# Performance work log

Hardware: AMD Instinct MI355X
Metric: run time of the kernel (lower is better)

The kernel has to match this reference:

```python
import jax, jax.numpy as jnp
import numpy as np

D_MODEL = 1024
D_FF = 4096
N_EXPERTS = 8
TOP_K = 2

def setup_inputs() -> dict:
    key = jax.random.key(0)
    ks = jax.random.split(key, 8)
    s = 0.02
    return {
        "x": jax.random.normal(ks[0], (4, 2048, D_MODEL), dtype=jnp.float32),
        "W1": jax.random.normal(ks[1], (N_EXPERTS, D_MODEL, D_FF), dtype=jnp.float32) * s,
        "b1": jnp.zeros((N_EXPERTS, D_FF), dtype=jnp.float32),
        "W2": jax.random.normal(ks[2], (N_EXPERTS, D_FF, D_MODEL), dtype=jnp.float32) * s,
        "b2": jnp.zeros((N_EXPERTS, D_MODEL), dtype=jnp.float32),
        "Wg": jax.random.normal(ks[3], (D_MODEL, N_EXPERTS), dtype=jnp.float32) * s,
        "bg": jnp.zeros((N_EXPERTS,), dtype=jnp.float32),
    }

def reference(x, W1, b1, W2, b2, Wg, bg):
    B, S, D = x.shape
    # Gating network
    gate_logits = jnp.einsum('bsd,de->bse', x, Wg) + bg
    gate_probs = jax.nn.softmax(gate_logits, axis=-1)  # (B,S,E)
    # Top-k routing on softmax probs (matches torch.topk(F.softmax(logits)))
    top_k_probs, top_k_indices = jax.lax.top_k(gate_probs, TOP_K)  # (B,S,k)
    T = B * S
    x_flat = x.reshape(T, D)
    idx_flat = top_k_indices.reshape(T, TOP_K)
    prob_flat = top_k_probs.reshape(T, TOP_K)
    # Per-token combine weight for each expert: sum of top-k probs routed to it
    # combine[t, e] = sum_j prob_flat[t, j] * (idx_flat[t, j] == e)
    onehot = jax.nn.one_hot(idx_flat, N_EXPERTS, dtype=x.dtype)  # (T,k,E)
    combine = jnp.einsum('tk,tke->te', prob_flat, onehot)  # (T,E)
    out = jnp.zeros((T, D), dtype=x.dtype)
    for e in range(N_EXPERTS):  # static small loop over experts
        h = jax.nn.relu(x_flat @ W1[e] + b1[e])  # (T, d_ff)
        y = h @ W2[e] + b2[e]                    # (T, d_model)
        out = out + combine[:, e:e+1] * y
    return out.reshape(B, S, D), gate_probs
```

## Files before the change

kernel.cpp:

```cpp
#include <hip/hip_runtime.h>

#define D_MODEL 1024
#define D_FF    4096
#define N_EXP   8
#define BM 256
#define BN 256
#define BK 64

typedef __attribute__((ext_vector_type(8))) short bf16x8;
typedef __attribute__((ext_vector_type(4))) float f32x4;
typedef unsigned int u32;

__device__ __forceinline__ unsigned short f2bf(float f) {
  union { float f; unsigned u; } v; v.f = f;
  unsigned r = v.u + 0x7FFFu + ((v.u >> 16) & 1u);
  return (unsigned short)(r >> 16);
}

__device__ __forceinline__ void gl_lds16(const void* g, void* l) {
  __builtin_amdgcn_global_load_lds((const __attribute__((address_space(1))) u32*)g,
                                   (__attribute__((address_space(3))) u32*)l, 16, 0, 0);
}

__global__ void convert_x_kernel(const float* __restrict__ x,
                                 unsigned short* __restrict__ xb, int total8) {
  int i = blockIdx.x * blockDim.x + threadIdx.x;
  if (i >= total8) return;
  const float4* src = (const float4*)x + (size_t)i * 2;
  float4 a = src[0], b = src[1];
  ushort4 lo, hi;
  lo.x = f2bf(a.x); lo.y = f2bf(a.y); lo.z = f2bf(a.z); lo.w = f2bf(a.w);
  hi.x = f2bf(b.x); hi.y = f2bf(b.y); hi.z = f2bf(b.z); hi.w = f2bf(b.w);
  ushort4* dst = (ushort4*)xb + (size_t)i * 2;
  dst[0] = lo; dst[1] = hi;
}

__global__ __launch_bounds__(256)
void transpose_convert_kernel(const float* __restrict__ src, unsigned short* __restrict__ dst,
                              int Ksub, int Nsrc, int k0, int n0, int Nchunk,
                              unsigned long long eStride) {
  __shared__ unsigned short s[64][65];
  int e = blockIdx.z;
  int kb = blockIdx.x * 64, nb = blockIdx.y * 64;
  const float* se = src + (size_t)e * eStride;
  unsigned short* de = dst + (size_t)e * Nchunk * Ksub;
  int tid = threadIdx.x;
  int lk = tid >> 4, ln = (tid & 15) * 4;
  #pragma unroll
  for (int p = 0; p < 4; p++) {
    int k = lk + p * 16;
    float4 v = *(const float4*)(se + (size_t)(k0 + kb + k) * Nsrc + (n0 + nb + ln));
    s[ln + 0][k] = f2bf(v.x);
    s[ln + 1][k] = f2bf(v.y);
    s[ln + 2][k] = f2bf(v.z);
    s[ln + 3][k] = f2bf(v.w);
  }
  __syncthreads();
  #pragma unroll
  for (int c = 0; c < 2; c++) {
    int id = tid + c * 256;
    int n = id >> 3, kc = id & 7;
    unsigned short u[8];
    #pragma unroll
    for (int j = 0; j < 8; j++) u[j] = s[n][kc * 8 + j];
    *(uint4*)(de + (size_t)(nb + n) * Ksub + kb + kc * 8) = *(const uint4*)u;
  }
}

__global__ void gating_kernel(const float* __restrict__ x,
                              const float* __restrict__ Wg,
                              const float* __restrict__ bg,
                              float* __restrict__ gate_out,
                              int* __restrict__ cnt,
                              int* __restrict__ tokIdx,
                              float* __restrict__ tokW, int T) {
  int wv = threadIdx.x >> 6, lane = threadIdx.x & 63;
  int t = blockIdx.x * 4 + wv;
  if (t >= T) return;
  const float* xr = x + (size_t)t * D_MODEL + lane * 16;
  float acc[N_EXP];
  #pragma unroll
  for (int e = 0; e < N_EXP; e++) acc[e] = 0.f;
  #pragma unroll
  for (int q = 0; q < 4; q++) {
    float4 xv = *(const float4*)(xr + q * 4);
    #pragma unroll
    for (int r = 0; r < 4; r++) {
      float xs = ((const float*)&xv)[r];
      const float* wrow = Wg + (size_t)(lane * 16 + q * 4 + r) * N_EXP;
      float4 wa = *(const float4*)wrow;
      float4 wb = *(const float4*)(wrow + 4);
      acc[0] += xs * wa.x; acc[1] += xs * wa.y; acc[2] += xs * wa.z; acc[3] += xs * wa.w;
      acc[4] += xs * wb.x; acc[5] += xs * wb.y; acc[6] += xs * wb.z; acc[7] += xs * wb.w;
    }
  }
  #pragma unroll
  for (int off = 32; off > 0; off >>= 1) {
    #pragma unroll
    for (int e = 0; e < N_EXP; e++) acc[e] += __shfl_xor(acc[e], off);
  }
  if (lane == 0) {
    float l[N_EXP], p[N_EXP];
    float m = -1e30f;
    #pragma unroll
    for (int e = 0; e < N_EXP; e++) { l[e] = acc[e] + bg[e]; m = fmaxf(m, l[e]); }
    float s = 0.f;
    #pragma unroll
    for (int e = 0; e < N_EXP; e++) { p[e] = __expf(l[e] - m); s += p[e]; }
    float inv = 1.f / s;
    #pragma unroll
    for (int e = 0; e < N_EXP; e++) { p[e] *= inv; gate_out[(size_t)t * N_EXP + e] = p[e]; }
    int e1 = 0;
    #pragma unroll
    for (int e = 1; e < N_EXP; e++) if (p[e] > p[e1]) e1 = e;
    int e2 = (e1 == 0) ? 1 : 0;
    #pragma unroll
    for (int e = 0; e < N_EXP; e++) if (e != e1 && p[e] > p[e2]) e2 = e;
    int pos = atomicAdd(cnt + e1, 1);
    tokIdx[(size_t)e1 * T + pos] = t; tokW[(size_t)e1 * T + pos] = p[e1];
    pos = atomicAdd(cnt + e2, 1);
    tokIdx[(size_t)e2 * T + pos] = t; tokW[(size_t)e2 * T + pos] = p[e2];
  }
}

__global__ void schedule_kernel(const int* __restrict__ cnt, int* __restrict__ meta,
                                int* __restrict__ tE, int* __restrict__ tB,
                                int* __restrict__ tV, int T, int maxTiles) {
  if (threadIdx.x != 0 || blockIdx.x != 0) return;
  int t = 0;
  for (int e = 0; e < N_EXP; e++) {
    int c = cnt[e];
    for (int r = 0; r < c && t < maxTiles; r += BM) {
      tE[t] = e; tB[t] = e * T + r; tV[t] = min(BM, c - r); t++;
    }
  }
  meta[0] = t;
}

#define STAGE(bufbase, kt) do { \
    _Pragma("unroll") for (int c_ = 0; c_ < 4; c_++) { \
      gl_lds16(srcA[c_] + (size_t)(kt) * BK, (bufbase) + (w * 32 + c_ * 8) * 64); \
      gl_lds16(srcB[c_] + (size_t)(kt) * BK, (bufbase) + 16384 + (w * 32 + c_ * 8) * 64); } \
  } while (0)

#define RD_A(cur, qm) { _Pragma("unroll") for (int m_ = 0; m_ < 4; m_++) { \
    int row_ = (qm) * 128 + wm64 + m_ * 16 + l15; \
    _Pragma("unroll") for (int kk_ = 0; kk_ < 2; kk_++) \
      a[m_][kk_] = *(const bf16x8*)&(cur)[row_ * 64 + (((kk_ * 4 + l4 + row_) & 7) << 3)]; } }

#define RD_B(cur, qn, bb) { _Pragma("unroll") for (int n_ = 0; n_ < 2; n_++) { \
    int rb_ = (qn) * 128 + wn32 + n_ * 16 + l15; \
    _Pragma("unroll") for (int kk_ = 0; kk_ < 2; kk_++) \
      bb[n_][kk_] = *(const bf16x8*)&(cur)[16384 + rb_ * 64 + (((kk_ * 4 + l4 + rb_) & 7) << 3)]; } }

#define MQ(qm, qn, bb) { _Pragma("unroll") for (int m_ = 0; m_ < 4; m_++) \
    _Pragma("unroll") for (int n_ = 0; n_ < 2; n_++) { \
      acc[qm][qn][m_][n_] = __builtin_amdgcn_mfma_f32_16x16x32_bf16(a[m_][0], bb[n_][0], acc[qm][qn][m_][n_], 0, 0, 0); \
      acc[qm][qn][m_][n_] = __builtin_amdgcn_mfma_f32_16x16x32_bf16(a[m_][1], bb[n_][1], acc[qm][qn][m_][n_], 0, 0, 0); } }

#define KLOOP(NT) \
  STAGE(As, 0); \
  asm volatile("s_waitcnt vmcnt(0)" ::: "memory"); \
  __builtin_amdgcn_sched_barrier(0); \
  __builtin_amdgcn_s_barrier(); \
  __builtin_amdgcn_sched_barrier(0); \
  for (int kt = 0; kt < (NT); kt++) { \
    unsigned short* cur = As + (kt & 1) * 32768; \
    unsigned short* nxt = As + ((kt + 1) & 1) * 32768; \
    if (kt + 1 < (NT)) STAGE(nxt, kt + 1); \
    __builtin_amdgcn_sched_barrier(0); \
    RD_A(cur, 0); RD_B(cur, 0, b0); RD_B(cur, 1, b1); \
    MQ(0, 0, b0); MQ(0, 1, b1); \
    RD_A(cur, 1); \
    MQ(1, 1, b1); MQ(1, 0, b0); \
    __builtin_amdgcn_sched_barrier(0); \
    asm volatile("s_waitcnt vmcnt(0)" ::: "memory"); \
    __builtin_amdgcn_sched_barrier(0); \
    __builtin_amdgcn_s_barrier(); \
    __builtin_amdgcn_sched_barrier(0); \
  }

#define ACC_INIT() f32x4 acc[2][2][4][2]; \
  _Pragma("unroll") for (int qm = 0; qm < 2; qm++) \
    _Pragma("unroll") for (int qn = 0; qn < 2; qn++) \
      _Pragma("unroll") for (int m = 0; m < 4; m++) \
        _Pragma("unroll") for (int n = 0; n < 2; n++) acc[qm][qn][m][n] = (f32x4){0.f, 0.f, 0.f, 0.f};

__global__ __launch_bounds__(512, 2)
void gemm1_kernel(const unsigned short* __restrict__ xb,
                  const unsigned short* __restrict__ w1t,
                  const float* __restrict__ b1,
                  const int* __restrict__ meta,
                  const int* __restrict__ tE, const int* __restrict__ tB,
                  const int* __restrict__ tV, const int* __restrict__ tokIdx,
                  unsigned short* __restrict__ hbuf, int FFC, int chunk_off, int ncolLog2) {
  __shared__ unsigned short As[65536];

  int total = gridDim.x;
  int L = blockIdx.x;
  int q = total >> 3, r8 = total & 7;
  int xcd = L & 7, idx = L >> 3;
  int work = (xcd < r8) ? (xcd * (q + 1) + idx) : (r8 * (q + 1) + (xcd - r8) * q + idx);
  int ncol = 1 << ncolLog2;
  int tile = work >> ncolLog2;
  int cb = work & (ncol - 1);
  if (tile >= meta[0]) return;
  int e = tE[tile], base = tB[tile], valid = tV[tile];
  int tid = threadIdx.x;

  int w = tid >> 6, lane = tid & 63;
  int wm = w >> 2, wn = w & 3;
  int wm64 = wm * 64, wn32 = wn * 32;
  int l15 = lane & 15, l4 = lane >> 4;
  int sr = lane >> 3, scg = lane & 7;

  const unsigned short* panel = w1t + (size_t)e * FFC * D_MODEL;
  const unsigned short* srcA[4];
  const unsigned short* srcB[4];
  #pragma unroll
  for (int c = 0; c < 4; c++) {
    int r = w * 32 + c * 8 + sr;
    int rc = r < valid ? r : valid - 1;
    int tok = tokIdx[base + rc];
    int swz = ((scg - r) & 7) << 3;
    srcA[c] = xb + (size_t)tok * D_MODEL + swz;
    srcB[c] = panel + (size_t)(cb * BN + r) * D_MODEL + swz;
  }

  ACC_INIT();
  bf16x8 a[4][2], b0[2][2], b1f[2][2];
  #define b1 b1f
  KLOOP(D_MODEL / BK);
  #undef b1

  const float* b1e = b1 + (size_t)e * D_FF + chunk_off + cb * BN;
  #pragma unroll
  for (int qn = 0; qn < 2; qn++)
    #pragma unroll
    for (int n = 0; n < 2; n++) {
      int colL = qn * 128 + wn32 + n * 16 + l15;
      float bias = b1e[colL];
      #pragma unroll
      for (int qm = 0; qm < 2; qm++)
        #pragma unroll
        for (int m = 0; m < 4; m++)
          #pragma unroll
          for (int r = 0; r < 4; r++) {
            int row = qm * 128 + wm64 + m * 16 + l4 * 4 + r;
            float v = acc[qm][qn][m][n][r] + bias;
            v = v > 0.f ? v : 0.f;
            hbuf[(size_t)(tile * BM + row) * FFC + cb * BN + colL] = f2bf(v);
          }
    }
}

__global__ __launch_bounds__(512, 2)
void gemm2_kernel(const unsigned short* __restrict__ hbuf,
                  const unsigned short* __restrict__ w2t,
                  const float* __restrict__ b2,
                  const int* __restrict__ meta,
                  const int* __restrict__ tE, const int* __restrict__ tB,
                  const int* __restrict__ tV, const int* __restrict__ tokIdx,
                  const float* __restrict__ tokW,
                  float* __restrict__ out, int FFC, int chunk) {
  __shared__ unsigned short As[65536];

  int total = gridDim.x;
  int L = blockIdx.x;
  int q = total >> 3, r8 = total & 7;
  int xcd = L & 7, idx = L >> 3;
  int work = (xcd < r8) ? (xcd * (q + 1) + idx) : (r8 * (q + 1) + (xcd - r8) * q + idx);
  int tile = work >> 3;
  int cb = (work >> 1) & 3;
  int ks = work & 1;
  if (tile >= meta[0]) return;
  int e = tE[tile], base = tB[tile], valid = tV[tile];
  int tid = threadIdx.x;

  int w = tid >> 6, lane = tid & 63;
  int wm = w >> 2, wn = w & 3;
  int wm64 = wm * 64, wn32 = wn * 32;
  int l15 = lane & 15, l4 = lane >> 4;
  int sr = lane >> 3, scg = lane & 7;

  const int nt = FFC / BK / 2;
  const int ksOff = ks * nt * BK;

  const unsigned short* panel = w2t + (size_t)e * D_MODEL * FFC;
  const unsigned short* srcA[4];
  const unsigned short* srcB[4];
  #pragma unroll
  for (int c = 0; c < 4; c++) {
    int r = w * 32 + c * 8 + sr;
    int swz = ((scg - r) & 7) << 3;
    srcA[c] = hbuf + (size_t)(tile * BM + r) * FFC + ksOff + swz;
    srcB[c] = panel + (size_t)(cb * BN + r) * FFC + ksOff + swz;
  }

  ACC_INIT();
  bf16x8 a[4][2], b0[2][2], b1[2][2];
  KLOOP(nt);

  int addBias = (chunk == 0 && ks == 0) ? 1 : 0;
  #pragma unroll
  for (int qn = 0; qn < 2; qn++)
    #pragma unroll
    for (int n = 0; n < 2; n++) {
      int colg = cb * BN + qn * 128 + wn32 + n * 16 + l15;
      float bias = addBias ? b2[(size_t)e * D_MODEL + colg] : 0.f;
      #pragma unroll
      for (int qm = 0; qm < 2; qm++)
        #pragma unroll
        for (int m = 0; m < 4; m++)
          #pragma unroll
          for (int r = 0; r < 4; r++) {
            int row = qm * 128 + wm64 + m * 16 + l4 * 4 + r;
            if (row < valid) {
              float wgt = tokW[base + row];
              int tok = tokIdx[base + row];
              float v = (acc[qm][qn][m][n][r] + bias) * wgt;
              atomicAdd(out + (size_t)tok * D_MODEL + colg, v);
            }
          }
    }
}

extern "C" void kernel_launch(void* const* d_in, const int* in_sizes, int n_in,
                              void* d_out, int out_size, void* d_ws, size_t ws_size,
                              hipStream_t stream) {
  const float* x  = (const float*)d_in[0];
  const float* W1 = (const float*)d_in[1];
  const float* b1 = (const float*)d_in[2];
  const float* W2 = (const float*)d_in[3];
  const float* b2 = (const float*)d_in[4];
  const float* Wg = (const float*)d_in[5];
  const float* bg = (const float*)d_in[6];

  int T = in_sizes[0] / D_MODEL;
  float* out = (float*)d_out;
  float* gate_out = out + (size_t)T * D_MODEL;

  char* ws = (char*)d_ws;
  int* cnt  = (int*)(ws + 0);
  int* meta = (int*)(ws + 64);
  int* tE   = (int*)(ws + 128);
  int* tB   = (int*)(ws + 1024);
  int* tV   = (int*)(ws + 2048);
  size_t off = 4096;
  int* tokIdx = (int*)(ws + off);   off += (size_t)N_EXP * T * 4;
  float* tokW = (float*)(ws + off); off += (size_t)N_EXP * T * 4;
  unsigned short* xb = (unsigned short*)(ws + off); off += (size_t)T * D_MODEL * 2;
  off = (off + 255) & ~(size_t)255;

  int maxTiles = (2 * T) / BM + N_EXP;
  int FFC = D_FF;
  while (FFC > 256 &&
         off + (size_t)FFC * (16384 + 16384 + (size_t)maxTiles * BM * 2) > ws_size)
    FFC >>= 1;

  unsigned short* w1t = (unsigned short*)(ws + off); off += (size_t)FFC * 16384;
  unsigned short* w2t = (unsigned short*)(ws + off); off += (size_t)FFC * 16384;
  unsigned short* h   = (unsigned short*)(ws + off);

  hipMemsetAsync(d_out, 0, (size_t)T * D_MODEL * sizeof(float), stream);
  hipMemsetAsync(cnt, 0, N_EXP * sizeof(int), stream);

  int total8 = T * D_MODEL / 8;
  convert_x_kernel<<<(total8 + 255) / 256, 256, 0, stream>>>(x, xb, total8);
  gating_kernel<<<(T + 3) / 4, 256, 0, stream>>>(x, Wg, bg, gate_out, cnt, tokIdx, tokW, T);
  schedule_kernel<<<1, 64, 0, stream>>>(cnt, meta, tE, tB, tV, T, maxTiles);

  int ncol1 = FFC / BN;
  int ncol1Log2 = __builtin_ctz(ncol1);
  for (int c = 0; c * FFC < D_FF; c++) {
    transpose_convert_kernel<<<dim3(D_MODEL / 64, FFC / 64, N_EXP), 256, 0, stream>>>(
        W1, w1t, D_MODEL, D_FF, 0, c * FFC, FFC, (unsigned long long)D_MODEL * D_FF);
    transpose_convert_kernel<<<dim3(FFC / 64, D_MODEL / 64, N_EXP), 256, 0, stream>>>(
        W2, w2t, FFC, D_MODEL, c * FFC, 0, D_MODEL, (unsigned long long)D_FF * D_MODEL);
    gemm1_kernel<<<maxTiles * ncol1, 512, 0, stream>>>(
        xb, w1t, b1, meta, tE, tB, tV, tokIdx, h, FFC, c * FFC, ncol1Log2);
    gemm2_kernel<<<maxTiles * (D_MODEL / BN) * 2, 512, 0, stream>>>(
        h, w2t, b2, meta, tE, tB, tV, tokIdx, tokW, out, FFC, c);
  }
}
```

Baseline: 836.2 us.

## Fuse x conversion into gating, repack transpose, split-K 4 in gemm2, tweak scheduling

Folds the fp32-to-bf16 conversion of x into the gating kernel so x is read once, and removes a launch. The weight transpose now packs pairs of bf16 into 32-bit LDS words to cut LDS traffic. gemm2 splits K four ways instead of two and caches token indices and weights in LDS. The K loops drop sched_barriers in favour of s_setprio, and launch bounds move to one block per CU. More split-K means more atomic adds to the output, and the lower occupancy hint may change register allocation.

```diff
diff --git a/kernel.cpp b/kernel.cpp
--- a/kernel.cpp
+++ b/kernel.cpp
@@ -22,48 +22,41 @@
                                    (__attribute__((address_space(3))) u32*)l, 16, 0, 0);
 }
 
-__global__ void convert_x_kernel(const float* __restrict__ x,
-                                 unsigned short* __restrict__ xb, int total8) {
-  int i = blockIdx.x * blockDim.x + threadIdx.x;
-  if (i >= total8) return;
-  const float4* src = (const float4*)x + (size_t)i * 2;
-  float4 a = src[0], b = src[1];
-  ushort4 lo, hi;
-  lo.x = f2bf(a.x); lo.y = f2bf(a.y); lo.z = f2bf(a.z); lo.w = f2bf(a.w);
-  hi.x = f2bf(b.x); hi.y = f2bf(b.y); hi.z = f2bf(b.z); hi.w = f2bf(b.w);
-  ushort4* dst = (ushort4*)xb + (size_t)i * 2;
-  dst[0] = lo; dst[1] = hi;
-}
-
 __global__ __launch_bounds__(256)
 void transpose_convert_kernel(const float* __restrict__ src, unsigned short* __restrict__ dst,
                               int Ksub, int Nsrc, int k0, int n0, int Nchunk,
                               unsigned long long eStride) {
-  __shared__ unsigned short s[64][65];
+  __shared__ u32 s32k[32][65];
   int e = blockIdx.z;
   int kb = blockIdx.x * 64, nb = blockIdx.y * 64;
-  const float* se = src + (size_t)e * eStride;
-  unsigned short* de = dst + (size_t)e * Nchunk * Ksub;
+  const float* se = src + (size_t)e * eStride + (size_t)(k0 + kb) * Nsrc + (n0 + nb);
+  unsigned short* de = dst + (size_t)e * Nchunk * Ksub + (size_t)nb * Ksub + kb;
   int tid = threadIdx.x;
-  int lk = tid >> 4, ln = (tid & 15) * 4;
-  #pragma unroll
-  for (int p = 0; p < 4; p++) {
-    int k = lk + p * 16;
-    float4 v = *(const float4*)(se + (size_t)(k0 + kb + k) * Nsrc + (n0 + nb + ln));
-    s[ln + 0][k] = f2bf(v.x);
-    s[ln + 1][k] = f2bf(v.y);
-    s[ln + 2][k] = f2bf(v.z);
-    s[ln + 3][k] = f2bf(v.w);
+  int kh = tid >> 4;
+  int n4 = (tid & 15) * 4;
+  #pragma unroll
+  for (int p = 0; p < 2; p++) {
+    int k = kh * 2 + p * 32;
+    float4 v0 = *(const float4*)(se + (size_t)k * Nsrc + n4);
+    float4 v1 = *(const float4*)(se + (size_t)(k + 1) * Nsrc + n4);
+    #pragma unroll
+    for (int j = 0; j < 4; j++) {
+      u32 pk = (u32)f2bf(((const float*)&v0)[j]) |
+               ((u32)f2bf(((const float*)&v1)[j]) << 16);
+      s32k[k >> 1][n4 + j] = pk;
+    }
   }
   __syncthreads();
   #pragma unroll
   for (int c = 0; c < 2; c++) {
     int id = tid + c * 256;
     int n = id >> 3, kc = id & 7;
-    unsigned short u[8];
-    #pragma unroll
-    for (int j = 0; j < 8; j++) u[j] = s[n][kc * 8 + j];
-    *(uint4*)(de + (size_t)(nb + n) * Ksub + kb + kc * 8) = *(const uint4*)u;
+    uint4 o;
+    o.x = s32k[kc * 4 + 0][n];
+    o.y = s32k[kc * 4 + 1][n];
+    o.z = s32k[kc * 4 + 2][n];
+    o.w = s32k[kc * 4 + 3][n];
+    *(uint4*)(de + (size_t)n * Ksub + kc * 8) = o;
   }
 }
 
@@ -71,6 +64,7 @@
                               const float* __restrict__ Wg,
                               const float* __restrict__ bg,
                               float* __restrict__ gate_out,
+                              unsigned short* __restrict__ xb,
                               int* __restrict__ cnt,
                               int* __restrict__ tokIdx,
                               float* __restrict__ tokW, int T) {
@@ -81,9 +75,12 @@
   float acc[N_EXP];
   #pragma unroll
   for (int e = 0; e < N_EXP; e++) acc[e] = 0.f;
+  ushort4 xc[4];
   #pragma unroll
   for (int q = 0; q < 4; q++) {
     float4 xv = *(const float4*)(xr + q * 4);
+    xc[q].x = f2bf(xv.x); xc[q].y = f2bf(xv.y);
+    xc[q].z = f2bf(xv.z); xc[q].w = f2bf(xv.w);
     #pragma unroll
     for (int r = 0; r < 4; r++) {
       float xs = ((const float*)&xv)[r];
@@ -94,6 +91,9 @@
       acc[4] += xs * wb.x; acc[5] += xs * wb.y; acc[6] += xs * wb.z; acc[7] += xs * wb.w;
     }
   }
+  unsigned short* xbr = xb + (size_t)t * D_MODEL + lane * 16;
+  #pragma unroll
+  for (int q = 0; q < 4; q++) *(ushort4*)(xbr + q * 4) = xc[q];
   #pragma unroll
   for (int off = 32; off > 0; off >>= 1) {
     #pragma unroll
@@ -161,23 +161,21 @@
 #define KLOOP(NT) \
   STAGE(As, 0); \
   asm volatile("s_waitcnt vmcnt(0)" ::: "memory"); \
-  __builtin_amdgcn_sched_barrier(0); \
   __builtin_amdgcn_s_barrier(); \
-  __builtin_amdgcn_sched_barrier(0); \
+  asm volatile("" ::: "memory"); \
   for (int kt = 0; kt < (NT); kt++) { \
     unsigned short* cur = As + (kt & 1) * 32768; \
     unsigned short* nxt = As + ((kt + 1) & 1) * 32768; \
     if (kt + 1 < (NT)) STAGE(nxt, kt + 1); \
-    __builtin_amdgcn_sched_barrier(0); \
-    RD_A(cur, 0); RD_B(cur, 0, b0); RD_B(cur, 1, b1); \
-    MQ(0, 0, b0); MQ(0, 1, b1); \
+    __builtin_amdgcn_s_setprio(1); \
+    RD_A(cur, 0); RD_B(cur, 0, rb0); RD_B(cur, 1, rb1); \
+    MQ(0, 0, rb0); MQ(0, 1, rb1); \
     RD_A(cur, 1); \
-    MQ(1, 1, b1); MQ(1, 0, b0); \
-    __builtin_amdgcn_sched_barrier(0); \
+    MQ(1, 1, rb1); MQ(1, 0, rb0); \
+    __builtin_amdgcn_s_setprio(0); \
     asm volatile("s_waitcnt vmcnt(0)" ::: "memory"); \
-    __builtin_amdgcn_sched_barrier(0); \
     __builtin_amdgcn_s_barrier(); \
-    __builtin_amdgcn_sched_barrier(0); \
+    asm volatile("" ::: "memory"); \
   }
 
 #define ACC_INIT() f32x4 acc[2][2][4][2]; \
@@ -186,10 +184,10 @@
       _Pragma("unroll") for (int m = 0; m < 4; m++) \
         _Pragma("unroll") for (int n = 0; n < 2; n++) acc[qm][qn][m][n] = (f32x4){0.f, 0.f, 0.f, 0.f};
 
-__global__ __launch_bounds__(512, 2)
+__global__ __launch_bounds__(512, 1)
 void gemm1_kernel(const unsigned short* __restrict__ xb,
                   const unsigned short* __restrict__ w1t,
-                  const float* __restrict__ b1,
+                  const float* __restrict__ bias1,
                   const int* __restrict__ meta,
                   const int* __restrict__ tE, const int* __restrict__ tB,
                   const int* __restrict__ tV, const int* __restrict__ tokIdx,
@@ -228,12 +226,10 @@
   }
 
   ACC_INIT();
-  bf16x8 a[4][2], b0[2][2], b1f[2][2];
-  #define b1 b1f
+  bf16x8 a[4][2], rb0[2][2], rb1[2][2];
   KLOOP(D_MODEL / BK);
-  #undef b1
-
-  const float* b1e = b1 + (size_t)e * D_FF + chunk_off + cb * BN;
+
+  const float* b1e = bias1 + (size_t)e * D_FF + chunk_off + cb * BN;
   #pragma unroll
   for (int qn = 0; qn < 2; qn++)
     #pragma unroll
@@ -254,28 +250,36 @@
     }
 }
 
-__global__ __launch_bounds__(512, 2)
+__global__ __launch_bounds__(512, 1)
 void gemm2_kernel(const unsigned short* __restrict__ hbuf,
                   const unsigned short* __restrict__ w2t,
-                  const float* __restrict__ b2,
+                  const float* __restrict__ bias2,
                   const int* __restrict__ meta,
                   const int* __restrict__ tE, const int* __restrict__ tB,
                   const int* __restrict__ tV, const int* __restrict__ tokIdx,
                   const float* __restrict__ tokW,
                   float* __restrict__ out, int FFC, int chunk) {
   __shared__ unsigned short As[65536];
+  __shared__ int stok[BM];
+  __shared__ float swt[BM];
 
   int total = gridDim.x;
   int L = blockIdx.x;
   int q = total >> 3, r8 = total & 7;
   int xcd = L & 7, idx = L >> 3;
   int work = (xcd < r8) ? (xcd * (q + 1) + idx) : (r8 * (q + 1) + (xcd - r8) * q + idx);
-  int tile = work >> 3;
-  int cb = (work >> 1) & 3;
-  int ks = work & 1;
+  int tile = work >> 4;
+  int cb = (work >> 2) & 3;
+  int ks = work & 3;
   if (tile >= meta[0]) return;
   int e = tE[tile], base = tB[tile], valid = tV[tile];
   int tid = threadIdx.x;
+
+  if (tid < BM) {
+    int rr = tid < valid ? tid : valid - 1;
+    stok[tid] = tokIdx[base + rr];
+    swt[tid] = tokW[base + rr];
+  }
 
   int w = tid >> 6, lane = tid & 63;
   int wm = w >> 2, wn = w & 3;
@@ -283,7 +287,7 @@
   int l15 = lane & 15, l4 = lane >> 4;
   int sr = lane >> 3, scg = lane & 7;
 
-  const int nt = FFC / BK / 2;
+  const int nt = FFC / BK / 4;
   const int ksOff = ks * nt * BK;
 
   const unsigned short* panel = w2t + (size_t)e * D_MODEL * FFC;
@@ -298,7 +302,7 @@
   }
 
   ACC_INIT();
-  bf16x8 a[4][2], b0[2][2], b1[2][2];
+  bf16x8 a[4][2], rb0[2][2], rb1[2][2];
   KLOOP(nt);
 
   int addBias = (chunk == 0 && ks == 0) ? 1 : 0;
@@ -307,7 +311,7 @@
     #pragma unroll
     for (int n = 0; n < 2; n++) {
       int colg = cb * BN + qn * 128 + wn32 + n * 16 + l15;
-      float bias = addBias ? b2[(size_t)e * D_MODEL + colg] : 0.f;
+      float bias = addBias ? bias2[(size_t)e * D_MODEL + colg] : 0.f;
       #pragma unroll
       for (int qm = 0; qm < 2; qm++)
         #pragma unroll
@@ -316,10 +320,8 @@
           for (int r = 0; r < 4; r++) {
             int row = qm * 128 + wm64 + m * 16 + l4 * 4 + r;
             if (row < valid) {
-              float wgt = tokW[base + row];
-              int tok = tokIdx[base + row];
-              float v = (acc[qm][qn][m][n][r] + bias) * wgt;
-              atomicAdd(out + (size_t)tok * D_MODEL + colg, v);
+              float v = (acc[qm][qn][m][n][r] + bias) * swt[row];
+              atomicAdd(out + (size_t)stok[row] * D_MODEL + colg, v);
             }
           }
     }
@@ -365,9 +367,7 @@
   hipMemsetAsync(d_out, 0, (size_t)T * D_MODEL * sizeof(float), stream);
   hipMemsetAsync(cnt, 0, N_EXP * sizeof(int), stream);
 
-  int total8 = T * D_MODEL / 8;
-  convert_x_kernel<<<(total8 + 255) / 256, 256, 0, stream>>>(x, xb, total8);
-  gating_kernel<<<(T + 3) / 4, 256, 0, stream>>>(x, Wg, bg, gate_out, cnt, tokIdx, tokW, T);
+  gating_kernel<<<(T + 3) / 4, 256, 0, stream>>>(x, Wg, bg, gate_out, xb, cnt, tokIdx, tokW, T);
   schedule_kernel<<<1, 64, 0, stream>>>(cnt, meta, tE, tB, tV, T, maxTiles);
 
   int ncol1 = FFC / BN;
@@ -379,7 +379,7 @@
         W2, w2t, FFC, D_MODEL, c * FFC, 0, D_MODEL, (unsigned long long)D_FF * D_MODEL);
     gemm1_kernel<<<maxTiles * ncol1, 512, 0, stream>>>(
         xb, w1t, b1, meta, tE, tB, tV, tokIdx, h, FFC, c * FFC, ncol1Log2);
-    gemm2_kernel<<<maxTiles * (D_MODEL / BN) * 2, 512, 0, stream>>>(
+    gemm2_kernel<<<maxTiles * 4 * 4, 512, 0, stream>>>(
         h, w2t, b2, meta, tE, tB, tV, tokIdx, tokW, out, FFC, c);
   }
 }
```

Measured after the change: 952.3 us. 13.9% more time.
